# Optimization experiments

Hardware: AMD Instinct MI355X
Metric: run time of the kernel (lower is better)

Reference implementation:

```python
import jax, jax.numpy as jnp
import numpy as np


def setup_inputs() -> dict:
    key = jax.random.key(0)
    kq, kk, kv = jax.random.split(key, 3)
    B, S, D = 16, 2048, 128
    q = jax.random.normal(kq, (B, S, D), dtype=jnp.float32)
    k = jax.random.normal(kk, (B, S, D), dtype=jnp.float32)
    v = jax.random.normal(kv, (B, S, D), dtype=jnp.float32)
    return {"q": q, "k": k, "v": v}


def reference(q, k, v):
    # scores = q @ k^T * scale  (scale = 1/sqrt(head_dim), the standard value
    # passed to this module; dropout=0.0 and attn_mask=None per defaults)
    scale = q.shape[-1] ** -0.5
    scores = jnp.einsum('bqd,bkd->bqk', q, k) * scale  # [B, S, S]
    attention = jax.nn.softmax(scores, axis=-1)
    context = jnp.einsum('bqk,bkd->bqd', attention, v)  # [B, S, D]
    return (context, attention)
```

## Files before the change

### kernel.cpp

```cpp
#include <hip/hip_runtime.h>

#define SS 2048
#define DD 128
#define NB 16
#define TM 64
#define TN 64
#define NITER (SS / TN)

typedef short bf16x8 __attribute__((ext_vector_type(8)));
typedef float f32x4 __attribute__((ext_vector_type(4)));

#define KSTRIDE 136
#define VSTRIDE 72
#define PSTRIDE 72

#define SL2E (0.08838834764831845f * 1.4426950408889634f)

__device__ __forceinline__ unsigned short f2bf(float x) {
    unsigned u = __builtin_bit_cast(unsigned, x);
    u += 0x7fffu + ((u >> 16) & 1u);
    return (unsigned short)(u >> 16);
}

__device__ __forceinline__ float fexp2(float x) {
#if __has_builtin(__builtin_amdgcn_exp2f)
    return __builtin_amdgcn_exp2f(x);
#else
    return __expf(x * 0.6931471805599453f);
#endif
}

__global__ void prep_kernel(const float* __restrict__ k, const float* __restrict__ v,
                            unsigned short* __restrict__ kb, unsigned short* __restrict__ vt) {
    __shared__ unsigned short t[64 * 72];
    const int x = blockIdx.x, b = blockIdx.z, sb = blockIdx.y * 64;
    const int tid = threadIdx.x;
    if (x < 2) {
        const int db = x * 64;
        const int r16 = tid >> 4, c4 = (tid & 15) * 4;
        for (int i = 0; i < 4; ++i) {
            int sl = i * 16 + r16;
            float4 xx = *(const float4*)(v + ((size_t)(b * SS + sb + sl) * DD + db + c4));
            ushort4 u; u.x = f2bf(xx.x); u.y = f2bf(xx.y); u.z = f2bf(xx.z); u.w = f2bf(xx.w);
            *(ushort4*)&t[sl * 72 + c4] = u;
        }
        __syncthreads();
        for (int i = 0; i < 4; ++i) {
            int dl = i * 16 + r16;
            ushort4 u;
            u.x = t[(c4 + 0) * 72 + dl];
            u.y = t[(c4 + 1) * 72 + dl];
            u.z = t[(c4 + 2) * 72 + dl];
            u.w = t[(c4 + 3) * 72 + dl];
            *(ushort4*)(vt + ((size_t)(b * DD + db + dl) * SS + sb + c4)) = u;
        }
    } else {
        const int c0 = (x - 2) * 64;
        for (int i = 0; i < 4; ++i) {
            int e = i * 1024 + tid * 4;
            int r = e >> 6, c = e & 63;
            size_t off = (size_t)(b * SS + sb + r) * DD + c0 + c;
            float4 xx = *(const float4*)(k + off);
            ushort4 u; u.x = f2bf(xx.x); u.y = f2bf(xx.y); u.z = f2bf(xx.z); u.w = f2bf(xx.w);
            *(ushort4*)(kb + off) = u;
        }
    }
}

__global__ __launch_bounds__(512, 4)
void attn_kernel(const float* __restrict__ q,
                 const unsigned short* __restrict__ kb,
                 const unsigned short* __restrict__ vt,
                 float* __restrict__ attn, float* __restrict__ ctx) {
    __shared__ unsigned short K_lds[TN * KSTRIDE];
    __shared__ unsigned short V_lds[DD * VSTRIDE];
    __shared__ unsigned short P_lds[TM * PSTRIDE];
    __shared__ float rs_lds[TM];
    __shared__ float inv_lds[TM];

    const int tid = threadIdx.x;
    const int lane = tid & 63, w = tid >> 6;
    const int wm = w >> 2, wn = w & 3;
    const int l15 = lane & 15, quad = lane >> 4;

    const int bid = blockIdx.x;
    const int bb = ((bid & 7) << 1) | ((bid >> 3) & 1);
    const int q0 = (bid >> 4) * TM;

    if (tid < TM) rs_lds[tid] = 0.0f;

    bf16x8 qf[2][4];
    {
        const float* qg = q + ((size_t)(bb * SS + q0 + wm * 32 + l15)) * DD + quad * 8;
        for (int mi = 0; mi < 2; ++mi)
            for (int kk = 0; kk < 4; ++kk) {
                float4 a = *(const float4*)(qg + mi * 16 * DD + kk * 32);
                float4 b = *(const float4*)(qg + mi * 16 * DD + kk * 32 + 4);
                bf16x8 f;
                f[0] = (short)f2bf(a.x); f[1] = (short)f2bf(a.y);
                f[2] = (short)f2bf(a.z); f[3] = (short)f2bf(a.w);
                f[4] = (short)f2bf(b.x); f[5] = (short)f2bf(b.y);
                f[6] = (short)f2bf(b.z); f[7] = (short)f2bf(b.w);
                qf[mi][kk] = f;
            }
    }

    const unsigned short* kgb = kb + (size_t)bb * SS * DD;
    const unsigned short* vgb = vt + (size_t)bb * DD * SS;

    float rs[8];
    for (int j = 0; j < 8; ++j) rs[j] = 0.0f;

    for (int it = 0; it < NITER; ++it) {
        __syncthreads();
        {
            const unsigned short* kg = kgb + (size_t)(it * TN) * DD;
            for (int c = 0; c < 2; ++c) {
                int e = c * 4096 + tid * 8;
                *(bf16x8*)&K_lds[(e >> 7) * KSTRIDE + (e & 127)] = *(const bf16x8*)(kg + e);
            }
        }
        __syncthreads();
        f32x4 acc[2];
        acc[0] = (f32x4){0.f, 0.f, 0.f, 0.f};
        acc[1] = (f32x4){0.f, 0.f, 0.f, 0.f};
        for (int kk = 0; kk < 4; ++kk) {
            bf16x8 bfv = *(const bf16x8*)&K_lds[(wn * 16 + l15) * KSTRIDE + kk * 32 + quad * 8];
            for (int mi = 0; mi < 2; ++mi)
                acc[mi] = __builtin_amdgcn_mfma_f32_16x16x32_bf16(qf[mi][kk], bfv, acc[mi], 0, 0, 0);
        }
        for (int mi = 0; mi < 2; ++mi)
            for (int r = 0; r < 4; ++r)
                rs[mi * 4 + r] += fexp2(acc[mi][r] * SL2E);
    }

    for (int j = 0; j < 8; ++j) {
        float s = rs[j];
        s += __shfl_xor(s, 1, 64);
        s += __shfl_xor(s, 2, 64);
        s += __shfl_xor(s, 4, 64);
        s += __shfl_xor(s, 8, 64);
        rs[j] = s;
    }
    if (l15 == 0)
        for (int mi = 0; mi < 2; ++mi)
            for (int r = 0; r < 4; ++r)
                atomicAdd(&rs_lds[wm * 32 + mi * 16 + quad * 4 + r], rs[mi * 4 + r]);
    __syncthreads();
    if (tid < TM) inv_lds[tid] = 1.0f / rs_lds[tid];
    __syncthreads();
    float inv[8];
    for (int mi = 0; mi < 2; ++mi)
        for (int r = 0; r < 4; ++r)
            inv[mi * 4 + r] = inv_lds[wm * 32 + mi * 16 + quad * 4 + r];

    f32x4 cacc[2][2];
    for (int mi = 0; mi < 2; ++mi)
        for (int ni = 0; ni < 2; ++ni) cacc[mi][ni] = (f32x4){0.f, 0.f, 0.f, 0.f};

    float* ap[8];
    for (int mi = 0; mi < 2; ++mi)
        for (int r = 0; r < 4; ++r)
            ap[mi * 4 + r] = attn + (size_t)bb * SS * SS
                           + (size_t)(q0 + wm * 32 + mi * 16 + quad * 4 + r) * SS
                           + wn * 16 + l15;

    for (int it = 0; it < NITER; ++it) {
        const int k0 = it * TN;
        __syncthreads();
        {
            const unsigned short* kg = kgb + (size_t)k0 * DD;
            for (int c = 0; c < 2; ++c) {
                int e = c * 4096 + tid * 8;
                *(bf16x8*)&K_lds[(e >> 7) * KSTRIDE + (e & 127)] = *(const bf16x8*)(kg + e);
            }
            const unsigned short* vg = vgb + k0;
            for (int c = 0; c < 2; ++c) {
                int e = c * 4096 + tid * 8;
                int dr = e >> 6, ck = e & 63;
                *(bf16x8*)&V_lds[dr * VSTRIDE + ck] = *(const bf16x8*)(vg + (size_t)dr * SS + ck);
            }
        }
        __syncthreads();

        f32x4 acc[2];
        acc[0] = (f32x4){0.f, 0.f, 0.f, 0.f};
        acc[1] = (f32x4){0.f, 0.f, 0.f, 0.f};
        for (int kk = 0; kk < 4; ++kk) {
            bf16x8 bfv = *(const bf16x8*)&K_lds[(wn * 16 + l15) * KSTRIDE + kk * 32 + quad * 8];
            for (int mi = 0; mi < 2; ++mi)
                acc[mi] = __builtin_amdgcn_mfma_f32_16x16x32_bf16(qf[mi][kk], bfv, acc[mi], 0, 0, 0);
        }

        for (int mi = 0; mi < 2; ++mi)
            for (int r = 0; r < 4; ++r) {
                float p = fexp2(acc[mi][r] * SL2E) * inv[mi * 4 + r];
                ap[mi * 4 + r][0] = p;
                P_lds[(wm * 32 + mi * 16 + quad * 4 + r) * PSTRIDE + wn * 16 + l15] = f2bf(p);
            }
        for (int j = 0; j < 8; ++j) ap[j] += TN;
        __syncthreads();

        for (int kk = 0; kk < 2; ++kk) {
            bf16x8 af[2];
            for (int mi = 0; mi < 2; ++mi)
                af[mi] = *(const bf16x8*)&P_lds[(wm * 32 + mi * 16 + l15) * PSTRIDE + kk * 32 + quad * 8];
            for (int ni = 0; ni < 2; ++ni) {
                bf16x8 bv = *(const bf16x8*)&V_lds[(wn * 32 + ni * 16 + l15) * VSTRIDE + kk * 32 + quad * 8];
                for (int mi = 0; mi < 2; ++mi)
                    cacc[mi][ni] = __builtin_amdgcn_mfma_f32_16x16x32_bf16(af[mi], bv, cacc[mi][ni], 0, 0, 0);
            }
        }
    }

    float* cg = ctx + ((size_t)(bb * SS) + q0) * DD;
    for (int mi = 0; mi < 2; ++mi)
        for (int ni = 0; ni < 2; ++ni)
            for (int r = 0; r < 4; ++r) {
                int row = wm * 32 + mi * 16 + quad * 4 + r;
                int col = wn * 32 + ni * 16 + l15;
                cg[(size_t)row * DD + col] = cacc[mi][ni][r];
            }
}

extern "C" void kernel_launch(void* const* d_in, const int* in_sizes, int n_in,
                              void* d_out, int out_size, void* d_ws, size_t ws_size,
                              hipStream_t stream) {
    const float* q = (const float*)d_in[0];
    const float* k = (const float*)d_in[1];
    const float* v = (const float*)d_in[2];
    float* ctx = (float*)d_out;
    float* attn = ctx + (size_t)NB * SS * DD;

    unsigned short* kb = (unsigned short*)d_ws;
    unsigned short* vt = kb + (size_t)NB * SS * DD;

    prep_kernel<<<dim3(4, SS / 64, NB), 256, 0, stream>>>(k, v, kb, vt);
    attn_kernel<<<dim3((SS / TM) * NB), 512, 0, stream>>>(q, kb, vt, attn, ctx);
}
```

Measured before the change: 371.8 us.

## Load K and V fragments directly from global into registers, double-buffer P

Removes the K and V shared-memory staging and each wave loads its MFMA operand fragments straight from global memory (relying on L1/L2 for reuse across waves). P is double-buffered in LDS so only one barrier per iteration is needed instead of three. Attention probability stores are deferred until after the PV MFMAs to overlap them with compute. This trades LDS traffic and barriers for redundant global/L2 loads across waves sharing the same K/V tiles.

```diff
diff --git a/kernel.cpp b/kernel.cpp
--- a/kernel.cpp
+++ b/kernel.cpp
@@ -6,15 +6,12 @@
 #define TM 64
 #define TN 64
 #define NITER (SS / TN)
+#define PSTRIDE 72
+
+#define SL2E (0.08838834764831845f * 1.4426950408889634f)
 
 typedef short bf16x8 __attribute__((ext_vector_type(8)));
 typedef float f32x4 __attribute__((ext_vector_type(4)));
-
-#define KSTRIDE 136
-#define VSTRIDE 72
-#define PSTRIDE 72
-
-#define SL2E (0.08838834764831845f * 1.4426950408889634f)
 
 __device__ __forceinline__ unsigned short f2bf(float x) {
     unsigned u = __builtin_bit_cast(unsigned, x);
@@ -72,9 +69,7 @@
                  const unsigned short* __restrict__ kb,
                  const unsigned short* __restrict__ vt,
                  float* __restrict__ attn, float* __restrict__ ctx) {
-    __shared__ unsigned short K_lds[TN * KSTRIDE];
-    __shared__ unsigned short V_lds[DD * VSTRIDE];
-    __shared__ unsigned short P_lds[TM * PSTRIDE];
+    __shared__ unsigned short P_lds[2][TM * PSTRIDE];
     __shared__ float rs_lds[TM];
     __shared__ float inv_lds[TM];
 
@@ -105,29 +100,22 @@
             }
     }
 
-    const unsigned short* kgb = kb + (size_t)bb * SS * DD;
+    const unsigned short* kfb = kb + (size_t)bb * SS * DD + (size_t)(wn * 16 + l15) * DD + quad * 8;
     const unsigned short* vgb = vt + (size_t)bb * DD * SS;
 
     float rs[8];
     for (int j = 0; j < 8; ++j) rs[j] = 0.0f;
 
     for (int it = 0; it < NITER; ++it) {
-        __syncthreads();
-        {
-            const unsigned short* kg = kgb + (size_t)(it * TN) * DD;
-            for (int c = 0; c < 2; ++c) {
-                int e = c * 4096 + tid * 8;
-                *(bf16x8*)&K_lds[(e >> 7) * KSTRIDE + (e & 127)] = *(const bf16x8*)(kg + e);
-            }
-        }
-        __syncthreads();
+        const unsigned short* kg = kfb + (size_t)(it * TN) * DD;
         f32x4 acc[2];
         acc[0] = (f32x4){0.f, 0.f, 0.f, 0.f};
         acc[1] = (f32x4){0.f, 0.f, 0.f, 0.f};
+        bf16x8 kf[4];
+        for (int kk = 0; kk < 4; ++kk) kf[kk] = *(const bf16x8*)(kg + kk * 32);
         for (int kk = 0; kk < 4; ++kk) {
-            bf16x8 bfv = *(const bf16x8*)&K_lds[(wn * 16 + l15) * KSTRIDE + kk * 32 + quad * 8];
-            for (int mi = 0; mi < 2; ++mi)
-                acc[mi] = __builtin_amdgcn_mfma_f32_16x16x32_bf16(qf[mi][kk], bfv, acc[mi], 0, 0, 0);
+            acc[0] = __builtin_amdgcn_mfma_f32_16x16x32_bf16(qf[0][kk], kf[kk], acc[0], 0, 0, 0);
+            acc[1] = __builtin_amdgcn_mfma_f32_16x16x32_bf16(qf[1][kk], kf[kk], acc[1], 0, 0, 0);
         }
         for (int mi = 0; mi < 2; ++mi)
             for (int r = 0; r < 4; ++r)
@@ -165,51 +153,49 @@
                            + (size_t)(q0 + wm * 32 + mi * 16 + quad * 4 + r) * SS
                            + wn * 16 + l15;
 
+    const unsigned short* vfb = vgb + (size_t)(wn * 32 + l15) * SS + quad * 8;
+
     for (int it = 0; it < NITER; ++it) {
         const int k0 = it * TN;
-        __syncthreads();
-        {
-            const unsigned short* kg = kgb + (size_t)k0 * DD;
-            for (int c = 0; c < 2; ++c) {
-                int e = c * 4096 + tid * 8;
-                *(bf16x8*)&K_lds[(e >> 7) * KSTRIDE + (e & 127)] = *(const bf16x8*)(kg + e);
-            }
-            const unsigned short* vg = vgb + k0;
-            for (int c = 0; c < 2; ++c) {
-                int e = c * 4096 + tid * 8;
-                int dr = e >> 6, ck = e & 63;
-                *(bf16x8*)&V_lds[dr * VSTRIDE + ck] = *(const bf16x8*)(vg + (size_t)dr * SS + ck);
-            }
-        }
-        __syncthreads();
-
+
+        bf16x8 vf[2][2];
+        for (int ni = 0; ni < 2; ++ni)
+            for (int kk = 0; kk < 2; ++kk)
+                vf[ni][kk] = *(const bf16x8*)(vfb + (size_t)(ni * 16) * SS + k0 + kk * 32);
+
+        const unsigned short* kg = kfb + (size_t)k0 * DD;
         f32x4 acc[2];
         acc[0] = (f32x4){0.f, 0.f, 0.f, 0.f};
         acc[1] = (f32x4){0.f, 0.f, 0.f, 0.f};
+        bf16x8 kf[4];
+        for (int kk = 0; kk < 4; ++kk) kf[kk] = *(const bf16x8*)(kg + kk * 32);
         for (int kk = 0; kk < 4; ++kk) {
-            bf16x8 bfv = *(const bf16x8*)&K_lds[(wn * 16 + l15) * KSTRIDE + kk * 32 + quad * 8];
-            for (int mi = 0; mi < 2; ++mi)
-                acc[mi] = __builtin_amdgcn_mfma_f32_16x16x32_bf16(qf[mi][kk], bfv, acc[mi], 0, 0, 0);
-        }
-
+            acc[0] = __builtin_amdgcn_mfma_f32_16x16x32_bf16(qf[0][kk], kf[kk], acc[0], 0, 0, 0);
+            acc[1] = __builtin_amdgcn_mfma_f32_16x16x32_bf16(qf[1][kk], kf[kk], acc[1], 0, 0, 0);
+        }
+
+        unsigned short* pb = P_lds[it & 1];
+        float pv[8];
         for (int mi = 0; mi < 2; ++mi)
             for (int r = 0; r < 4; ++r) {
                 float p = fexp2(acc[mi][r] * SL2E) * inv[mi * 4 + r];
-                ap[mi * 4 + r][0] = p;
-                P_lds[(wm * 32 + mi * 16 + quad * 4 + r) * PSTRIDE + wn * 16 + l15] = f2bf(p);
+                pv[mi * 4 + r] = p;
+                pb[(wm * 32 + mi * 16 + quad * 4 + r) * PSTRIDE + wn * 16 + l15] = f2bf(p);
             }
-        for (int j = 0; j < 8; ++j) ap[j] += TN;
         __syncthreads();
 
         for (int kk = 0; kk < 2; ++kk) {
             bf16x8 af[2];
             for (int mi = 0; mi < 2; ++mi)
-                af[mi] = *(const bf16x8*)&P_lds[(wm * 32 + mi * 16 + l15) * PSTRIDE + kk * 32 + quad * 8];
-            for (int ni = 0; ni < 2; ++ni) {
-                bf16x8 bv = *(const bf16x8*)&V_lds[(wn * 32 + ni * 16 + l15) * VSTRIDE + kk * 32 + quad * 8];
+                af[mi] = *(const bf16x8*)&pb[(wm * 32 + mi * 16 + l15) * PSTRIDE + kk * 32 + quad * 8];
+            for (int ni = 0; ni < 2; ++ni)
                 for (int mi = 0; mi < 2; ++mi)
-                    cacc[mi][ni] = __builtin_amdgcn_mfma_f32_16x16x32_bf16(af[mi], bv, cacc[mi][ni], 0, 0, 0);
-            }
+                    cacc[mi][ni] = __builtin_amdgcn_mfma_f32_16x16x32_bf16(af[mi], vf[ni][kk], cacc[mi][ni], 0, 0, 0);
+        }
+
+        for (int j = 0; j < 8; ++j) {
+            ap[j][0] = pv[j];
+            ap[j] += TN;
         }
     }
 
```

Result: slower. 470.7 us (+26.6%).

## Double the key tile, prefetch K through registers, and read V from global

Applied to the files above, without the earlier changes.

Doubles the key tile to 128 columns and replaces the separate K/V/P LDS arrays with one two-slot buffer. In the row-sum pass, the next K tile is prefetched into registers and stored into the alternate slot, so there is one barrier per iteration. In the output pass, V fragments come straight from global memory into registers, P is double-buffered in LDS, and the next K tile is loaded while the PV MFMAs run. The goal is fewer barriers and overlap of global loads with compute, at the cost of more LDS per block (lower occupancy) and more register pressure.

```diff
diff --git a/kernel.cpp b/kernel.cpp
--- a/kernel.cpp
+++ b/kernel.cpp
@@ -4,17 +4,15 @@
 #define DD 128
 #define NB 16
 #define TM 64
-#define TN 64
+#define TN 128
 #define NITER (SS / TN)
+#define KSTRIDE 136
+#define PSTRIDE 136
+
+#define SL2E (0.08838834764831845f * 1.4426950408889634f)
 
 typedef short bf16x8 __attribute__((ext_vector_type(8)));
 typedef float f32x4 __attribute__((ext_vector_type(4)));
-
-#define KSTRIDE 136
-#define VSTRIDE 72
-#define PSTRIDE 72
-
-#define SL2E (0.08838834764831845f * 1.4426950408889634f)
 
 __device__ __forceinline__ unsigned short f2bf(float x) {
     unsigned u = __builtin_bit_cast(unsigned, x);
@@ -72,9 +70,7 @@
                  const unsigned short* __restrict__ kb,
                  const unsigned short* __restrict__ vt,
                  float* __restrict__ attn, float* __restrict__ ctx) {
-    __shared__ unsigned short K_lds[TN * KSTRIDE];
-    __shared__ unsigned short V_lds[DD * VSTRIDE];
-    __shared__ unsigned short P_lds[TM * PSTRIDE];
+    __shared__ unsigned short smem[2][TN * KSTRIDE];
     __shared__ float rs_lds[TM];
     __shared__ float inv_lds[TM];
 
@@ -106,33 +102,49 @@
     }
 
     const unsigned short* kgb = kb + (size_t)bb * SS * DD;
-    const unsigned short* vgb = vt + (size_t)bb * DD * SS;
+
+    for (int c = 0; c < 4; ++c) {
+        int e = c * 4096 + tid * 8;
+        *(bf16x8*)&smem[0][(e >> 7) * KSTRIDE + (e & 127)] = *(const bf16x8*)(kgb + e);
+    }
+    __syncthreads();
 
     float rs[8];
     for (int j = 0; j < 8; ++j) rs[j] = 0.0f;
 
     for (int it = 0; it < NITER; ++it) {
-        __syncthreads();
-        {
-            const unsigned short* kg = kgb + (size_t)(it * TN) * DD;
-            for (int c = 0; c < 2; ++c) {
+        bf16x8 g[4];
+        if (it + 1 < NITER) {
+            const unsigned short* kg = kgb + (size_t)((it + 1) * TN) * DD;
+            for (int c = 0; c < 4; ++c)
+                g[c] = *(const bf16x8*)(kg + c * 4096 + tid * 8);
+        }
+        const unsigned short* kt = smem[it & 1];
+        f32x4 acc[2][2];
+        for (int mi = 0; mi < 2; ++mi)
+            for (int nt = 0; nt < 2; ++nt) acc[mi][nt] = (f32x4){0.f, 0.f, 0.f, 0.f};
+        for (int nt = 0; nt < 2; ++nt)
+            for (int kk = 0; kk < 4; ++kk) {
+                bf16x8 kf = *(const bf16x8*)&kt[(wn * 32 + nt * 16 + l15) * KSTRIDE + kk * 32 + quad * 8];
+                acc[0][nt] = __builtin_amdgcn_mfma_f32_16x16x32_bf16(qf[0][kk], kf, acc[0][nt], 0, 0, 0);
+                acc[1][nt] = __builtin_amdgcn_mfma_f32_16x16x32_bf16(qf[1][kk], kf, acc[1][nt], 0, 0, 0);
+            }
+        for (int mi = 0; mi < 2; ++mi)
+            for (int r = 0; r < 4; ++r)
+                rs[mi * 4 + r] += fexp2(acc[mi][0][r] * SL2E) + fexp2(acc[mi][1][r] * SL2E);
+        if (it + 1 < NITER) {
+            unsigned short* kd = smem[(it + 1) & 1];
+            for (int c = 0; c < 4; ++c) {
                 int e = c * 4096 + tid * 8;
-                *(bf16x8*)&K_lds[(e >> 7) * KSTRIDE + (e & 127)] = *(const bf16x8*)(kg + e);
-            }
-        }
-        __syncthreads();
-        f32x4 acc[2];
-        acc[0] = (f32x4){0.f, 0.f, 0.f, 0.f};
-        acc[1] = (f32x4){0.f, 0.f, 0.f, 0.f};
-        for (int kk = 0; kk < 4; ++kk) {
-            bf16x8 bfv = *(const bf16x8*)&K_lds[(wn * 16 + l15) * KSTRIDE + kk * 32 + quad * 8];
-            for (int mi = 0; mi < 2; ++mi)
-                acc[mi] = __builtin_amdgcn_mfma_f32_16x16x32_bf16(qf[mi][kk], bfv, acc[mi], 0, 0, 0);
-        }
-        for (int mi = 0; mi < 2; ++mi)
-            for (int r = 0; r < 4; ++r)
-                rs[mi * 4 + r] += fexp2(acc[mi][r] * SL2E);
-    }
+                *(bf16x8*)&kd[(e >> 7) * KSTRIDE + (e & 127)] = g[c];
+            }
+        }
+        __syncthreads();
+    }
+
+    bf16x8 g0[4];
+    for (int c = 0; c < 4; ++c)
+        g0[c] = *(const bf16x8*)(kgb + c * 4096 + tid * 8);
 
     for (int j = 0; j < 8; ++j) {
         float s = rs[j];
@@ -148,6 +160,10 @@
                 atomicAdd(&rs_lds[wm * 32 + mi * 16 + quad * 4 + r], rs[mi * 4 + r]);
     __syncthreads();
     if (tid < TM) inv_lds[tid] = 1.0f / rs_lds[tid];
+    for (int c = 0; c < 4; ++c) {
+        int e = c * 4096 + tid * 8;
+        *(bf16x8*)&smem[0][(e >> 7) * KSTRIDE + (e & 127)] = g0[c];
+    }
     __syncthreads();
     float inv[8];
     for (int mi = 0; mi < 2; ++mi)
@@ -158,59 +174,71 @@
     for (int mi = 0; mi < 2; ++mi)
         for (int ni = 0; ni < 2; ++ni) cacc[mi][ni] = (f32x4){0.f, 0.f, 0.f, 0.f};
 
-    float* ap[8];
-    for (int mi = 0; mi < 2; ++mi)
-        for (int r = 0; r < 4; ++r)
-            ap[mi * 4 + r] = attn + (size_t)bb * SS * SS
-                           + (size_t)(q0 + wm * 32 + mi * 16 + quad * 4 + r) * SS
-                           + wn * 16 + l15;
+    const unsigned short* vfb = vt + (size_t)bb * DD * SS + (size_t)(wn * 32 + l15) * SS + quad * 8;
+    float* apb = attn + (size_t)bb * SS * SS + (size_t)(q0 + wm * 32 + quad * 4) * SS + wn * 32 + l15;
 
     for (int it = 0; it < NITER; ++it) {
         const int k0 = it * TN;
-        __syncthreads();
-        {
-            const unsigned short* kg = kgb + (size_t)k0 * DD;
-            for (int c = 0; c < 2; ++c) {
-                int e = c * 4096 + tid * 8;
-                *(bf16x8*)&K_lds[(e >> 7) * KSTRIDE + (e & 127)] = *(const bf16x8*)(kg + e);
-            }
-            const unsigned short* vg = vgb + k0;
-            for (int c = 0; c < 2; ++c) {
-                int e = c * 4096 + tid * 8;
-                int dr = e >> 6, ck = e & 63;
-                *(bf16x8*)&V_lds[dr * VSTRIDE + ck] = *(const bf16x8*)(vg + (size_t)dr * SS + ck);
-            }
-        }
-        __syncthreads();
-
-        f32x4 acc[2];
-        acc[0] = (f32x4){0.f, 0.f, 0.f, 0.f};
-        acc[1] = (f32x4){0.f, 0.f, 0.f, 0.f};
-        for (int kk = 0; kk < 4; ++kk) {
-            bf16x8 bfv = *(const bf16x8*)&K_lds[(wn * 16 + l15) * KSTRIDE + kk * 32 + quad * 8];
-            for (int mi = 0; mi < 2; ++mi)
-                acc[mi] = __builtin_amdgcn_mfma_f32_16x16x32_bf16(qf[mi][kk], bfv, acc[mi], 0, 0, 0);
-        }
-
-        for (int mi = 0; mi < 2; ++mi)
-            for (int r = 0; r < 4; ++r) {
-                float p = fexp2(acc[mi][r] * SL2E) * inv[mi * 4 + r];
-                ap[mi * 4 + r][0] = p;
-                P_lds[(wm * 32 + mi * 16 + quad * 4 + r) * PSTRIDE + wn * 16 + l15] = f2bf(p);
-            }
-        for (int j = 0; j < 8; ++j) ap[j] += TN;
-        __syncthreads();
+
+        bf16x8 vf[2][2];
+        for (int ni = 0; ni < 2; ++ni)
+            for (int kk = 0; kk < 2; ++kk)
+                vf[ni][kk] = *(const bf16x8*)(vfb + ni * 16 * SS + k0 + kk * 32);
+
+        f32x4 acc[2][2];
+        for (int mi = 0; mi < 2; ++mi)
+            for (int nt = 0; nt < 2; ++nt) acc[mi][nt] = (f32x4){0.f, 0.f, 0.f, 0.f};
+        for (int nt = 0; nt < 2; ++nt)
+            for (int kk = 0; kk < 4; ++kk) {
+                bf16x8 kf = *(const bf16x8*)&smem[0][(wn * 32 + nt * 16 + l15) * KSTRIDE + kk * 32 + quad * 8];
+                acc[0][nt] = __builtin_amdgcn_mfma_f32_16x16x32_bf16(qf[0][kk], kf, acc[0][nt], 0, 0, 0);
+                acc[1][nt] = __builtin_amdgcn_mfma_f32_16x16x32_bf16(qf[1][kk], kf, acc[1][nt], 0, 0, 0);
+            }
+
+        unsigned short* pb = &smem[1][0] + (it & 1) * (TM * PSTRIDE);
+        for (int mi = 0; mi < 2; ++mi)
+            for (int nt = 0; nt < 2; ++nt)
+                for (int r = 0; r < 4; ++r) {
+                    float p = fexp2(acc[mi][nt][r] * SL2E) * inv[mi * 4 + r];
+                    pb[(wm * 32 + mi * 16 + quad * 4 + r) * PSTRIDE + wn * 32 + nt * 16 + l15] = f2bf(p);
+                    apb[(mi * 16 + r) * SS + k0 + nt * 16] = p;
+                }
+        __syncthreads();
+
+        bf16x8 g[4];
+        if (it + 1 < NITER) {
+            const unsigned short* kg = kgb + (size_t)((it + 1) * TN) * DD;
+            for (int c = 0; c < 4; ++c)
+                g[c] = *(const bf16x8*)(kg + c * 4096 + tid * 8);
+        }
 
         for (int kk = 0; kk < 2; ++kk) {
             bf16x8 af[2];
             for (int mi = 0; mi < 2; ++mi)
-                af[mi] = *(const bf16x8*)&P_lds[(wm * 32 + mi * 16 + l15) * PSTRIDE + kk * 32 + quad * 8];
-            for (int ni = 0; ni < 2; ++ni) {
-                bf16x8 bv = *(const bf16x8*)&V_lds[(wn * 32 + ni * 16 + l15) * VSTRIDE + kk * 32 + quad * 8];
+                af[mi] = *(const bf16x8*)&pb[(wm * 32 + mi * 16 + l15) * PSTRIDE + kk * 32 + quad * 8];
+            for (int ni = 0; ni < 2; ++ni)
                 for (int mi = 0; mi < 2; ++mi)
-                    cacc[mi][ni] = __builtin_amdgcn_mfma_f32_16x16x32_bf16(af[mi], bv, cacc[mi][ni], 0, 0, 0);
-            }
-        }
+                    cacc[mi][ni] = __builtin_amdgcn_mfma_f32_16x16x32_bf16(af[mi], vf[ni][kk], cacc[mi][ni], 0, 0, 0);
+        }
+        for (int ni = 0; ni < 2; ++ni)
+            for (int kk = 0; kk < 2; ++kk)
+                vf[ni][kk] = *(const bf16x8*)(vfb + ni * 16 * SS + k0 + (kk + 2) * 32);
+        for (int kk = 0; kk < 2; ++kk) {
+            bf16x8 af[2];
+            for (int mi = 0; mi < 2; ++mi)
+                af[mi] = *(const bf16x8*)&pb[(wm * 32 + mi * 16 + l15) * PSTRIDE + (kk + 2) * 32 + quad * 8];
+            for (int ni = 0; ni < 2; ++ni)
+                for (int mi = 0; mi < 2; ++mi)
+                    cacc[mi][ni] = __builtin_amdgcn_mfma_f32_16x16x32_bf16(af[mi], vf[ni][kk], cacc[mi][ni], 0, 0, 0);
+        }
+
+        if (it + 1 < NITER) {
+            for (int c = 0; c < 4; ++c) {
+                int e = c * 4096 + tid * 8;
+                *(bf16x8*)&smem[0][(e >> 7) * KSTRIDE + (e & 127)] = g[c];
+            }
+        }
+        __syncthreads();
     }
 
     float* cg = ctx + ((size_t)(bb * SS) + q0) * DD;
```

New measurement: 394.1 us. 6.0% more time.
